# Kernel tuning notes

Hardware: AMD Instinct MI355X
Metric: run time of the kernel (lower is better)

The kernel has to match this reference:

```python
import jax, jax.numpy as jnp
import numpy as np

D_MODEL = 768
D_INNER = 1536
D_STATE = 16
D_CONV = 4
DT_RANK = 48
BATCH = 1
SEQ = 2048


def setup_inputs() -> dict:
    key = jax.random.key(0)
    ks = jax.random.split(key, 8)
    s = 0.02
    x = jax.random.normal(ks[0], (BATCH, SEQ, D_MODEL), dtype=jnp.float32)
    W_in = jax.random.normal(ks[1], (2 * D_INNER, D_MODEL), dtype=jnp.float32) * s
    conv_w = jax.random.normal(ks[2], (D_INNER, 1, D_CONV), dtype=jnp.float32) * s
    conv_b = jnp.zeros((D_INNER,), dtype=jnp.float32)
    W_x = jax.random.normal(ks[3], (DT_RANK + 2 * D_STATE, D_INNER), dtype=jnp.float32) * s
    W_dt = jax.random.normal(ks[4], (D_INNER, DT_RANK), dtype=jnp.float32) * s
    b_dt = jax.random.normal(ks[5], (D_INNER,), dtype=jnp.float32) * s
    # A = arange(1, d_state+1) broadcast over d_inner; parameter is log(A)
    A_log = jnp.log(jnp.broadcast_to(jnp.arange(1, D_STATE + 1, dtype=jnp.float32), (D_INNER, D_STATE)))
    D_param = jnp.ones((D_INNER,), dtype=jnp.float32)
    W_out = jax.random.normal(ks[6], (D_MODEL, D_INNER), dtype=jnp.float32) * s
    return {"x": x, "W_in": W_in, "conv_w": conv_w, "conv_b": conv_b, "W_x": W_x,
            "W_dt": W_dt, "b_dt": b_dt, "A_log": A_log, "D_param": D_param, "W_out": W_out}


def _mamba_forward(x, W_in, conv_w, conv_b, W_x, W_dt, b_dt, A_log, D_param, W_out):
    B, L, _ = x.shape
    # in_proj and split into conv branch and gate
    xz = x @ W_in.T                              # [B, L, 2*d_inner]
    xb, z = jnp.split(xz, 2, axis=-1)
    # causal depthwise conv1d (padding=d_conv-1 then trim == left pad d_conv-1)
    xc = jnp.transpose(xb, (0, 2, 1))            # [B, d_inner, L]
    xc = jax.lax.conv_general_dilated(
        xc, conv_w, window_strides=(1,), padding=[(D_CONV - 1, 0)],
        feature_group_count=D_INNER, dimension_numbers=("NCH", "OIH", "NCH"))
    xc = xc + conv_b[None, :, None]
    xb = jax.nn.silu(jnp.transpose(xc, (0, 2, 1)))  # [B, L, d_inner]
    # input-dependent dt, B, C
    xdbl = xb @ W_x.T                            # [B, L, dt_rank + 2*d_state]
    dt = xdbl[..., :DT_RANK]
    Bm = xdbl[..., DT_RANK:DT_RANK + D_STATE]
    Cm = xdbl[..., DT_RANK + D_STATE:]
    dt = jax.nn.softplus(dt @ W_dt.T + b_dt)     # [B, L, d_inner]
    # discretize
    A = -jnp.exp(A_log)                          # [d_inner, d_state]
    dA = jnp.exp(jnp.einsum("bld,dn->bldn", dt, A))          # [B, L, d_inner, d_state]
    dBx = dt[..., None] * Bm[:, :, None, :] * xb[..., None]   # dB * x, [B, L, d_inner, d_state]
    # sequential scan: h[t] = dA[t]*h[t-1] + dBx[t]; y[t] = <h[t], C[t]>
    def step(h, inp):
        dA_t, dBx_t, C_t = inp
        h = dA_t * h + dBx_t                     # [B, d_inner, d_state]
        y_t = jnp.einsum("bdn,bn->bd", h, C_t)
        return h, y_t
    h0 = jnp.zeros((B, D_INNER, D_STATE), dtype=x.dtype)
    _, ys = jax.lax.scan(step, h0, (jnp.moveaxis(dA, 1, 0), jnp.moveaxis(dBx, 1, 0), jnp.moveaxis(Cm, 1, 0)))
    y = jnp.moveaxis(ys, 0, 1) + xb * D_param    # [B, L, d_inner]
    # gate and output projection
    y = y * jax.nn.silu(z)
    return y @ W_out.T                           # [B, L, d_model]


def reference(x, W_in, conv_w, conv_b, W_x, W_dt, b_dt, A_log, D_param, W_out):
    return _mamba_forward(x, W_in, conv_w, conv_b, W_x, W_dt, b_dt, A_log, D_param, W_out)
```

## Files before the change

### kernel.cpp

```cpp
#include <hip/hip_runtime.h>
#include <hip/hip_bf16.h>

#define D_MODEL 768
#define D_INNER 1536
#define D_STATE 16
#define DT_RANK 48
#define SEQ 2048
#define NC 32
#define LC (SEQ / NC)
#define DN (D_INNER * D_STATE)
#define KS 8
#define KCH (D_INNER / KS)

typedef float f32x4 __attribute__((ext_vector_type(4)));
typedef short bf16x8 __attribute__((ext_vector_type(8)));

typedef const __attribute__((address_space(1))) unsigned int* gas_u32;
typedef __attribute__((address_space(3))) unsigned int* las_u32;

__device__ __forceinline__ void gload16(const void* g, void* l) {
  __builtin_amdgcn_global_load_lds((gas_u32)g, (las_u32)l, 16, 0, 0);
}

__device__ __forceinline__ ushort f2bf_bits(float f) {
  uint u = __float_as_uint(f);
  u += 0x7FFFu + ((u >> 16) & 1u);
  return (ushort)(u >> 16);
}
__device__ __forceinline__ float bf_bits2f(ushort b) {
  return __uint_as_float(((uint)b) << 16);
}

__device__ __forceinline__ void split_vec4(const float* __restrict__ src,
                                           ushort* __restrict__ hi,
                                           ushort* __restrict__ lo, int idx) {
  const float4 v = ((const float4*)src)[idx];
  const float f[4] = {v.x, v.y, v.z, v.w};
  ushort4 h, l;
  ushort* hp = (ushort*)&h;
  ushort* lp = (ushort*)&l;
#pragma unroll
  for (int j = 0; j < 4; ++j) {
    const ushort hb = f2bf_bits(f[j]);
    hp[j] = hb;
    lp[j] = f2bf_bits(f[j] - bf_bits2f(hb));
  }
  ((ushort4*)hi)[idx] = h;
  ((ushort4*)lo)[idx] = l;
}

__global__ __launch_bounds__(256) void split3_bf16_kernel(
    const float* __restrict__ s0, ushort* __restrict__ h0, ushort* __restrict__ l0, int n0v,
    const float* __restrict__ s1, ushort* __restrict__ h1, ushort* __restrict__ l1, int n1v,
    const float* __restrict__ s2, ushort* __restrict__ h2, ushort* __restrict__ l2) {
  int idx = blockIdx.x * 256 + threadIdx.x;
  if (idx < n0v) {
    split_vec4(s0, h0, l0, idx);
  } else if (idx < n0v + n1v) {
    split_vec4(s1, h1, l1, idx - n0v);
  } else {
    split_vec4(s2, h2, l2, idx - n0v - n1v);
  }
}

template <int BM, int BN>
__global__ __launch_bounds__(256) void gemm_mfma_presplit(
    const ushort* __restrict__ Ah, const ushort* __restrict__ Al, int lda,
    const ushort* __restrict__ Bh, const ushort* __restrict__ Bl, int ldb,
    float* __restrict__ C, int ldc, int K) {
  __shared__ __align__(16) ushort As_hi[BM * 64];
  __shared__ __align__(16) ushort As_lo[BM * 64];
  __shared__ __align__(16) ushort Bs_hi[BN * 64];
  __shared__ __align__(16) ushort Bs_lo[BN * 64];

  const int tid = threadIdx.x;
  const int lane = tid & 63;
  const int wave = tid >> 6;
  const int wbase = tid & 192;
  const int m0 = blockIdx.y * BM;
  const int n0 = blockIdx.x * BN;

  constexpr int FM = BM / 32;
  constexpr int FN = BN / 32;
  const int wm0 = (wave >> 1) * (BM / 2);
  const int wn0 = (wave & 1) * (BN / 2);
  const int fr = lane & 15;
  const int kg = lane >> 4;

  f32x4 acc[FM][FN] = {};

  for (int k0 = 0; k0 < K; k0 += 64) {
#pragma unroll
    for (int i = 0; i < BM / 32; ++i) {
      const int slot = i * 256 + tid;
      const int row = slot >> 3;
      const int c8 = (slot & 7) << 3;
      const size_t g = (size_t)(m0 + row) * lda + k0 + c8;
      const int lb = (i * 256 + wbase) * 8;
      gload16(&Ah[g], &As_hi[lb]);
      gload16(&Al[g], &As_lo[lb]);
    }
#pragma unroll
    for (int i = 0; i < BN / 32; ++i) {
      const int slot = i * 256 + tid;
      const int row = slot >> 3;
      const int c8 = (slot & 7) << 3;
      const size_t g = (size_t)(n0 + row) * ldb + k0 + c8;
      const int lb = (i * 256 + wbase) * 8;
      gload16(&Bh[g], &Bs_hi[lb]);
      gload16(&Bl[g], &Bs_lo[lb]);
    }
    __syncthreads();

#pragma unroll
    for (int k2 = 0; k2 < 64; k2 += 32) {
      bf16x8 ah[FM], al[FM];
#pragma unroll
      for (int m = 0; m < FM; ++m) {
        const int base = (wm0 + m * 16 + fr) * 64 + k2 + kg * 8;
        ah[m] = *(const bf16x8*)&As_hi[base];
        al[m] = *(const bf16x8*)&As_lo[base];
      }
#pragma unroll
      for (int n = 0; n < FN; ++n) {
        const int base = (wn0 + n * 16 + fr) * 64 + k2 + kg * 8;
        const bf16x8 bh = *(const bf16x8*)&Bs_hi[base];
        const bf16x8 bl = *(const bf16x8*)&Bs_lo[base];
#pragma unroll
        for (int m = 0; m < FM; ++m) {
          acc[m][n] = __builtin_amdgcn_mfma_f32_16x16x32_bf16(ah[m], bh, acc[m][n], 0, 0, 0);
          acc[m][n] = __builtin_amdgcn_mfma_f32_16x16x32_bf16(ah[m], bl, acc[m][n], 0, 0, 0);
          acc[m][n] = __builtin_amdgcn_mfma_f32_16x16x32_bf16(al[m], bh, acc[m][n], 0, 0, 0);
        }
      }
    }
    __syncthreads();
  }

#pragma unroll
  for (int m = 0; m < FM; ++m) {
#pragma unroll
    for (int n = 0; n < FN; ++n) {
      const int row = m0 + wm0 + m * 16 + (lane >> 4) * 4;
      const int col = n0 + wn0 + n * 16 + (lane & 15);
#pragma unroll
      for (int r = 0; r < 4; ++r) C[(row + r) * ldc + col] = acc[m][n][r];
    }
  }
}

__global__ __launch_bounds__(256) void gemm2_splitk(
    const float* __restrict__ A,
    const float* __restrict__ B,
    float* __restrict__ part) {
  __shared__ __align__(16) float As[16][68];
  __shared__ __align__(16) float Bs[16][84];

  const int tid = threadIdx.x;
  const int tx = tid & 15;
  const int ty = tid >> 4;
  const int m0 = blockIdx.x * 64;
  const int kbase = blockIdx.y * KCH;

  float acc[4][5] = {};

  for (int k0 = 0; k0 < KCH; k0 += 16) {
    {
      const int am = tid >> 2;
      const int ak = (tid & 3) << 2;
      const float4 av = *(const float4*)&A[(m0 + am) * D_INNER + kbase + k0 + ak];
      As[ak + 0][am] = av.x;
      As[ak + 1][am] = av.y;
      As[ak + 2][am] = av.z;
      As[ak + 3][am] = av.w;
    }
    for (int f = tid; f < 80 * 4; f += 256) {
      const int row = f >> 2;
      const int kk = (f & 3) << 2;
      const float4 bv = *(const float4*)&B[row * D_INNER + kbase + k0 + kk];
      Bs[kk + 0][row] = bv.x;
      Bs[kk + 1][row] = bv.y;
      Bs[kk + 2][row] = bv.z;
      Bs[kk + 3][row] = bv.w;
    }
    __syncthreads();

#pragma unroll
    for (int k = 0; k < 16; ++k) {
      const float4 a4 = *(const float4*)&As[k][ty * 4];
      const float a[4] = {a4.x, a4.y, a4.z, a4.w};
      float b[5];
#pragma unroll
      for (int j = 0; j < 5; ++j) b[j] = Bs[k][tx + 16 * j];
#pragma unroll
      for (int i = 0; i < 4; ++i)
#pragma unroll
        for (int j = 0; j < 5; ++j) acc[i][j] = fmaf(a[i], b[j], acc[i][j]);
    }
    __syncthreads();
  }

  const int pb = (blockIdx.y * SEQ + m0) * 80;
#pragma unroll
  for (int i = 0; i < 4; ++i)
#pragma unroll
    for (int j = 0; j < 5; ++j)
      part[pb + (ty * 4 + i) * 80 + tx + 16 * j] = acc[i][j];
}

__global__ __launch_bounds__(256) void gemm2_reduce(
    const float* __restrict__ part, float* __restrict__ xdbl) {
  const int idx = blockIdx.x * 256 + threadIdx.x;
  float s = 0.f;
#pragma unroll
  for (int ks = 0; ks < KS; ++ks) s += part[ks * SEQ * 80 + idx];
  xdbl[idx] = s;
}

template <int MODE>
__global__ __launch_bounds__(256) void gemm_kernel(
    const float* __restrict__ A, int lda,
    const float* __restrict__ B, int ldb,
    const float* __restrict__ bias,
    float* __restrict__ C, int ldc,
    int M, int N, int K) {
  __shared__ __align__(16) float As[16][68];
  __shared__ __align__(16) float Bs[16][68];

  const int tid = threadIdx.x;
  const int tx = tid & 15;
  const int ty = tid >> 4;
  const int m0 = blockIdx.y * 64;
  const int n0 = blockIdx.x * 64;

  const int am = tid >> 2;
  const int ak = (tid & 3) << 2;

  float acc[4][4] = {};

  for (int k0 = 0; k0 < K; k0 += 16) {
    {
      const float4 av = *(const float4*)&A[(m0 + am) * lda + k0 + ak];
      As[ak + 0][am] = av.x;
      As[ak + 1][am] = av.y;
      As[ak + 2][am] = av.z;
      As[ak + 3][am] = av.w;
    }
    {
      const int bn = n0 + am;
      float4 bv = make_float4(0.f, 0.f, 0.f, 0.f);
      if (bn < N) bv = *(const float4*)&B[bn * ldb + k0 + ak];
      Bs[ak + 0][am] = bv.x;
      Bs[ak + 1][am] = bv.y;
      Bs[ak + 2][am] = bv.z;
      Bs[ak + 3][am] = bv.w;
    }
    __syncthreads();

#pragma unroll
    for (int k = 0; k < 16; ++k) {
      const float4 a = *(const float4*)&As[k][ty * 4];
      const float4 b = *(const float4*)&Bs[k][tx * 4];
      const float ar[4] = {a.x, a.y, a.z, a.w};
      const float br[4] = {b.x, b.y, b.z, b.w};
#pragma unroll
      for (int i = 0; i < 4; ++i)
#pragma unroll
        for (int j = 0; j < 4; ++j) acc[i][j] = fmaf(ar[i], br[j], acc[i][j]);
    }
    __syncthreads();
  }

#pragma unroll
  for (int i = 0; i < 4; ++i) {
    const int m = m0 + ty * 4 + i;
#pragma unroll
    for (int j = 0; j < 4; ++j) {
      const int n = n0 + tx * 4 + j;
      if (n < N) {
        float v = acc[i][j];
        if (MODE == 1) {
          v += bias[n];
          v = (v > 20.f) ? v : log1pf(__expf(v));
        }
        C[m * ldc + n] = v;
      }
    }
  }
}

__global__ __launch_bounds__(256) void conv_silu_kernel(
    const float* __restrict__ xz, const float* __restrict__ cw,
    const float* __restrict__ cb, float* __restrict__ xbc) {
  const int idx = blockIdx.x * 256 + threadIdx.x;
  const int t = idx / (D_INNER / 4);
  const int d = (idx - t * (D_INNER / 4)) * 4;
  const float4 w0 = *(const float4*)&cw[(d + 0) * 4];
  const float4 w1 = *(const float4*)&cw[(d + 1) * 4];
  const float4 w2 = *(const float4*)&cw[(d + 2) * 4];
  const float4 w3 = *(const float4*)&cw[(d + 3) * 4];
  float4 acc = *(const float4*)&cb[d];
#pragma unroll
  for (int j = 0; j < 4; ++j) {
    const int tt = t + j - 3;
    if (tt >= 0) {
      const float4 xv = *(const float4*)&xz[tt * (2 * D_INNER) + d];
      acc.x = fmaf(xv.x, ((const float*)&w0)[j], acc.x);
      acc.y = fmaf(xv.y, ((const float*)&w1)[j], acc.y);
      acc.z = fmaf(xv.z, ((const float*)&w2)[j], acc.z);
      acc.w = fmaf(xv.w, ((const float*)&w3)[j], acc.w);
    }
  }
  float4 r;
  r.x = acc.x / (1.f + __expf(-acc.x));
  r.y = acc.y / (1.f + __expf(-acc.y));
  r.z = acc.z / (1.f + __expf(-acc.z));
  r.w = acc.w / (1.f + __expf(-acc.w));
  *(float4*)&xbc[t * D_INNER + d] = r;
}

__global__ __launch_bounds__(256) void scan_part1(
    const float* __restrict__ dt, const float* __restrict__ xdbl,
    const float* __restrict__ xbc, const float* __restrict__ A_log,
    float* __restrict__ aprod, float* __restrict__ hloc) {
  __shared__ float dt_s[LC][16];
  __shared__ float xb_s[LC][16];
  __shared__ float B_s[LC][16];

  const int tid = threadIdx.x;
  const int ch = tid >> 4;
  const int n = tid & 15;
  const int d0 = blockIdx.x * 16;
  const int c = blockIdx.y;
  const int t0 = c * LC;

  for (int f = tid; f < LC * 16; f += 256) {
    const int t = f >> 4, cc = f & 15;
    const int gt = t0 + t;
    dt_s[t][cc] = dt[gt * D_INNER + d0 + cc];
    xb_s[t][cc] = xbc[gt * D_INNER + d0 + cc];
    B_s[t][cc] = xdbl[gt * 80 + DT_RANK + cc];
  }
  __syncthreads();

  const float Aval = -__expf(A_log[(d0 + ch) * D_STATE + n]);
  float h = 0.f, ap = 1.f;
#pragma unroll 4
  for (int t = 0; t < LC; ++t) {
    const float sdt = dt_s[t][ch];
    const float dA = __expf(sdt * Aval);
    h = fmaf(dA, h, sdt * B_s[t][n] * xb_s[t][ch]);
    ap *= dA;
  }
  const int idx = c * DN + d0 * 16 + tid;
  aprod[idx] = ap;
  hloc[idx] = h;
}

__global__ __launch_bounds__(256) void scan_combine(
    const float* __restrict__ aprod, const float* __restrict__ hloc,
    float* __restrict__ hstart) {
  const int idx = blockIdx.x * 256 + threadIdx.x;
  float hs = 0.f;
#pragma unroll
  for (int c = 0; c < NC; ++c) {
    const float a = aprod[c * DN + idx];
    const float hl = hloc[c * DN + idx];
    hstart[c * DN + idx] = hs;
    hs = fmaf(a, hs, hl);
  }
}

__global__ __launch_bounds__(256) void scan_part3(
    const float* __restrict__ dt, const float* __restrict__ xdbl,
    const float* __restrict__ xbc, const float* __restrict__ xz,
    const float* __restrict__ A_log, const float* __restrict__ Dp,
    const float* __restrict__ hstart,
    ushort* __restrict__ ym_hi, ushort* __restrict__ ym_lo) {
  __shared__ float dt_s[LC][16];
  __shared__ float xb_s[LC][16];
  __shared__ float z_s[LC][16];
  __shared__ float B_s[LC][16];
  __shared__ float C_s[LC][16];
  __shared__ float y_s[LC][16];

  const int tid = threadIdx.x;
  const int ch = tid >> 4;
  const int n = tid & 15;
  const int d0 = blockIdx.x * 16;
  const int c = blockIdx.y;
  const int t0 = c * LC;

  for (int f = tid; f < LC * 16; f += 256) {
    const int t = f >> 4, cc = f & 15;
    const int gt = t0 + t;
    dt_s[t][cc] = dt[gt * D_INNER + d0 + cc];
    xb_s[t][cc] = xbc[gt * D_INNER + d0 + cc];
    z_s[t][cc] = xz[gt * (2 * D_INNER) + D_INNER + d0 + cc];
    B_s[t][cc] = xdbl[gt * 80 + DT_RANK + cc];
    C_s[t][cc] = xdbl[gt * 80 + DT_RANK + D_STATE + cc];
  }
  __syncthreads();

  const float Aval = -__expf(A_log[(d0 + ch) * D_STATE + n]);
  const float Dval = Dp[d0 + ch];
  float h = hstart[c * DN + d0 * 16 + tid];

#pragma unroll 4
  for (int t = 0; t < LC; ++t) {
    const float sdt = dt_s[t][ch];
    const float bx = xb_s[t][ch];
    const float dA = __expf(sdt * Aval);
    h = fmaf(dA, h, sdt * B_s[t][n] * bx);
    float p = h * C_s[t][n];
    p += __shfl_xor(p, 1, 16);
    p += __shfl_xor(p, 2, 16);
    p += __shfl_xor(p, 4, 16);
    p += __shfl_xor(p, 8, 16);
    if (n == 0) {
      const float zz = z_s[t][ch];
      const float sig = 1.f / (1.f + __expf(-zz));
      y_s[t][ch] = (p + bx * Dval) * (zz * sig);
    }
  }
  __syncthreads();

  for (int f = tid; f < LC * 16; f += 256) {
    const int t = f >> 4, cc = f & 15;
    const float v = y_s[t][cc];
    const ushort hb = f2bf_bits(v);
    const int gidx = (t0 + t) * D_INNER + d0 + cc;
    ym_hi[gidx] = hb;
    ym_lo[gidx] = f2bf_bits(v - bf_bits2f(hb));
  }
}

extern "C" void kernel_launch(void* const* d_in, const int* in_sizes, int n_in,
                              void* d_out, int out_size, void* d_ws,
                              size_t ws_size, hipStream_t stream) {
  const float* x = (const float*)d_in[0];
  const float* W_in = (const float*)d_in[1];
  const float* conv_w = (const float*)d_in[2];
  const float* conv_b = (const float*)d_in[3];
  const float* W_x = (const float*)d_in[4];
  const float* W_dt = (const float*)d_in[5];
  const float* b_dt = (const float*)d_in[6];
  const float* A_log = (const float*)d_in[7];
  const float* D_param = (const float*)d_in[8];
  const float* W_out = (const float*)d_in[9];
  float* out = (float*)d_out;

  float* ws = (float*)d_ws;
  float* xz = ws;
  float* xbc = xz + SEQ * 2 * D_INNER;
  float* xdbl = xbc + SEQ * D_INNER;
  float* dtb = xdbl + SEQ * 80;
  float* aprod = dtb + SEQ * D_INNER;
  float* hloc = aprod + NC * DN;
  float* hstart = hloc + NC * DN;

  ushort* x_hi = (ushort*)(hstart + NC * DN);
  ushort* x_lo = x_hi + SEQ * D_MODEL;
  ushort* wi_hi = x_lo + SEQ * D_MODEL;
  ushort* wi_lo = wi_hi + 2 * D_INNER * D_MODEL;
  ushort* wo_hi = wi_lo + 2 * D_INNER * D_MODEL;
  ushort* wo_lo = wo_hi + D_MODEL * D_INNER;
  ushort* ym_hi = wo_lo + D_MODEL * D_INNER;
  ushort* ym_lo = ym_hi + SEQ * D_INNER;

  float* part = (float*)x_hi;

  const dim3 blk(256);

  const int n0v = SEQ * D_MODEL / 4;
  const int n1v = 2 * D_INNER * D_MODEL / 4;
  const int n2v = D_MODEL * D_INNER / 4;
  split3_bf16_kernel<<<dim3((n0v + n1v + n2v) / 256), blk, 0, stream>>>(
      x, x_hi, x_lo, n0v, W_in, wi_hi, wi_lo, n1v, W_out, wo_hi, wo_lo);

  gemm_mfma_presplit<128, 128><<<dim3(2 * D_INNER / 128, SEQ / 128), blk, 0, stream>>>(
      x_hi, x_lo, D_MODEL, wi_hi, wi_lo, D_MODEL, xz, 2 * D_INNER, D_MODEL);

  conv_silu_kernel<<<dim3(SEQ * D_INNER / 1024), blk, 0, stream>>>(
      xz, conv_w, conv_b, xbc);

  gemm2_splitk<<<dim3(SEQ / 64, KS), blk, 0, stream>>>(xbc, W_x, part);
  gemm2_reduce<<<dim3(SEQ * 80 / 256), blk, 0, stream>>>(part, xdbl);

  gemm_kernel<1><<<dim3(D_INNER / 64, SEQ / 64), blk, 0, stream>>>(
      xdbl, 80, W_dt, DT_RANK, b_dt, dtb, D_INNER, SEQ, D_INNER, DT_RANK);

  scan_part1<<<dim3(D_INNER / 16, NC), blk, 0, stream>>>(
      dtb, xdbl, xbc, A_log, aprod, hloc);
  scan_combine<<<dim3(DN / 256), blk, 0, stream>>>(aprod, hloc, hstart);
  scan_part3<<<dim3(D_INNER / 16, NC), blk, 0, stream>>>(
      dtb, xdbl, xbc, xz, A_log, D_param, hstart, ym_hi, ym_lo);

  gemm_mfma_presplit<64, 64><<<dim3(D_MODEL / 64, SEQ / 64), blk, 0, stream>>>(
      ym_hi, ym_lo, D_INNER, wo_hi, wo_lo, D_INNER, out, D_MODEL, D_INNER);
}
```

Baseline: 305.2 us.

## Transpose scan LDS tiles for vector reads, use DPP reduction, hoist gating

Both chunked-scan kernels now store dt, xb, B and C in shared memory transposed and padded to a row stride of 68. This lets each thread fetch four timesteps with a single float4 LDS read. In the output kernel, the 16-lane shuffle reduction over states is replaced by DPP row operations, which avoids the cost of cross-lane permutes. The SiLU gate and D skip term move out of the serial time loop into the vectorised write-back phase. This shortens the per-timestep critical path, in exchange for extra global reads of z in the epilogue and a layout with possible LDS bank conflicts on the transposed writes.

New measurement: 267.7 us. -12.3%, faster.

```diff
diff --git a/kernel.cpp b/kernel.cpp
--- a/kernel.cpp
+++ b/kernel.cpp
@@ -20,6 +20,19 @@
 
 __device__ __forceinline__ void gload16(const void* g, void* l) {
   __builtin_amdgcn_global_load_lds((gas_u32)g, (las_u32)l, 16, 0, 0);
+}
+
+__device__ __forceinline__ float dpp_radd16(float v) {
+  int x;
+  x = __builtin_amdgcn_update_dpp(0, __float_as_int(v), 0xB1, 0xF, 0xF, true);
+  v += __int_as_float(x);
+  x = __builtin_amdgcn_update_dpp(0, __float_as_int(v), 0x4E, 0xF, 0xF, true);
+  v += __int_as_float(x);
+  x = __builtin_amdgcn_update_dpp(0, __float_as_int(v), 0x141, 0xF, 0xF, true);
+  v += __int_as_float(x);
+  x = __builtin_amdgcn_update_dpp(0, __float_as_int(v), 0x140, 0xF, 0xF, true);
+  v += __int_as_float(x);
+  return v;
 }
 
 __device__ __forceinline__ ushort f2bf_bits(float f) {
@@ -323,9 +336,9 @@
     const float* __restrict__ dt, const float* __restrict__ xdbl,
     const float* __restrict__ xbc, const float* __restrict__ A_log,
     float* __restrict__ aprod, float* __restrict__ hloc) {
-  __shared__ float dt_s[LC][16];
-  __shared__ float xb_s[LC][16];
-  __shared__ float B_s[LC][16];
+  __shared__ __align__(16) float dt_s[16][68];
+  __shared__ __align__(16) float xb_s[16][68];
+  __shared__ __align__(16) float B_s[16][68];
 
   const int tid = threadIdx.x;
   const int ch = tid >> 4;
@@ -337,20 +350,25 @@
   for (int f = tid; f < LC * 16; f += 256) {
     const int t = f >> 4, cc = f & 15;
     const int gt = t0 + t;
-    dt_s[t][cc] = dt[gt * D_INNER + d0 + cc];
-    xb_s[t][cc] = xbc[gt * D_INNER + d0 + cc];
-    B_s[t][cc] = xdbl[gt * 80 + DT_RANK + cc];
+    dt_s[cc][t] = dt[gt * D_INNER + d0 + cc];
+    xb_s[cc][t] = xbc[gt * D_INNER + d0 + cc];
+    B_s[cc][t] = xdbl[gt * 80 + DT_RANK + cc];
   }
   __syncthreads();
 
   const float Aval = -__expf(A_log[(d0 + ch) * D_STATE + n]);
   float h = 0.f, ap = 1.f;
-#pragma unroll 4
-  for (int t = 0; t < LC; ++t) {
-    const float sdt = dt_s[t][ch];
-    const float dA = __expf(sdt * Aval);
-    h = fmaf(dA, h, sdt * B_s[t][n] * xb_s[t][ch]);
-    ap *= dA;
+  for (int t4 = 0; t4 < LC; t4 += 4) {
+    const float4 dtv = *(const float4*)&dt_s[ch][t4];
+    const float4 xbv = *(const float4*)&xb_s[ch][t4];
+    const float4 Bv = *(const float4*)&B_s[n][t4];
+#pragma unroll
+    for (int j = 0; j < 4; ++j) {
+      const float sdt = ((const float*)&dtv)[j];
+      const float dA = __expf(sdt * Aval);
+      h = fmaf(dA, h, sdt * ((const float*)&Bv)[j] * ((const float*)&xbv)[j]);
+      ap *= dA;
+    }
   }
   const int idx = c * DN + d0 * 16 + tid;
   aprod[idx] = ap;
@@ -377,11 +395,10 @@
     const float* __restrict__ A_log, const float* __restrict__ Dp,
     const float* __restrict__ hstart,
     ushort* __restrict__ ym_hi, ushort* __restrict__ ym_lo) {
-  __shared__ float dt_s[LC][16];
-  __shared__ float xb_s[LC][16];
-  __shared__ float z_s[LC][16];
-  __shared__ float B_s[LC][16];
-  __shared__ float C_s[LC][16];
+  __shared__ __align__(16) float dt_s[16][68];
+  __shared__ __align__(16) float xb_s[16][68];
+  __shared__ __align__(16) float B_s[16][68];
+  __shared__ __align__(16) float C_s[16][68];
   __shared__ float y_s[LC][16];
 
   const int tid = threadIdx.x;
@@ -394,42 +411,40 @@
   for (int f = tid; f < LC * 16; f += 256) {
     const int t = f >> 4, cc = f & 15;
     const int gt = t0 + t;
-    dt_s[t][cc] = dt[gt * D_INNER + d0 + cc];
-    xb_s[t][cc] = xbc[gt * D_INNER + d0 + cc];
-    z_s[t][cc] = xz[gt * (2 * D_INNER) + D_INNER + d0 + cc];
-    B_s[t][cc] = xdbl[gt * 80 + DT_RANK + cc];
-    C_s[t][cc] = xdbl[gt * 80 + DT_RANK + D_STATE + cc];
+    dt_s[cc][t] = dt[gt * D_INNER + d0 + cc];
+    xb_s[cc][t] = xbc[gt * D_INNER + d0 + cc];
+    B_s[cc][t] = xdbl[gt * 80 + DT_RANK + cc];
+    C_s[cc][t] = xdbl[gt * 80 + DT_RANK + D_STATE + cc];
   }
   __syncthreads();
 
   const float Aval = -__expf(A_log[(d0 + ch) * D_STATE + n]);
-  const float Dval = Dp[d0 + ch];
   float h = hstart[c * DN + d0 * 16 + tid];
 
-#pragma unroll 4
-  for (int t = 0; t < LC; ++t) {
-    const float sdt = dt_s[t][ch];
-    const float bx = xb_s[t][ch];
-    const float dA = __expf(sdt * Aval);
-    h = fmaf(dA, h, sdt * B_s[t][n] * bx);
-    float p = h * C_s[t][n];
-    p += __shfl_xor(p, 1, 16);
-    p += __shfl_xor(p, 2, 16);
-    p += __shfl_xor(p, 4, 16);
-    p += __shfl_xor(p, 8, 16);
-    if (n == 0) {
-      const float zz = z_s[t][ch];
-      const float sig = 1.f / (1.f + __expf(-zz));
-      y_s[t][ch] = (p + bx * Dval) * (zz * sig);
+  for (int t4 = 0; t4 < LC; t4 += 4) {
+    const float4 dtv = *(const float4*)&dt_s[ch][t4];
+    const float4 xbv = *(const float4*)&xb_s[ch][t4];
+    const float4 Bv = *(const float4*)&B_s[n][t4];
+    const float4 Cv = *(const float4*)&C_s[n][t4];
+#pragma unroll
+    for (int j = 0; j < 4; ++j) {
+      const float sdt = ((const float*)&dtv)[j];
+      const float dA = __expf(sdt * Aval);
+      h = fmaf(dA, h, sdt * ((const float*)&Bv)[j] * ((const float*)&xbv)[j]);
+      const float p = dpp_radd16(h * ((const float*)&Cv)[j]);
+      if (n == 0) y_s[t4 + j][ch] = p;
     }
   }
   __syncthreads();
 
   for (int f = tid; f < LC * 16; f += 256) {
     const int t = f >> 4, cc = f & 15;
-    const float v = y_s[t][cc];
+    const int gt = t0 + t;
+    const float zz = xz[gt * (2 * D_INNER) + D_INNER + d0 + cc];
+    const float sig = 1.f / (1.f + __expf(-zz));
+    const float v = (y_s[t][cc] + xb_s[cc][t] * Dp[d0 + cc]) * (zz * sig);
     const ushort hb = f2bf_bits(v);
-    const int gidx = (t0 + t) * D_INNER + d0 + cc;
+    const int gidx = gt * D_INNER + d0 + cc;
     ym_hi[gidx] = hb;
     ym_lo[gidx] = f2bf_bits(v - bf_bits2f(hb));
   }
```
